# Kernel optimization log

Hardware: AMD Instinct MI355X
Metric: run time of the kernel (lower is better)

The kernel has to match this reference:

```python
import jax, jax.numpy as jnp
import numpy as np

B, L, S, H, E, D = 4, 2048, 2048, 8, 64, 64

def setup_inputs() -> dict:
    key = jax.random.key(0)
    kq, kk, kv = jax.random.split(key, 3)
    queries = jax.random.normal(kq, (B, L, H, E), dtype=jnp.float32)
    keys = jax.random.normal(kk, (B, S, H, E), dtype=jnp.float32)
    values = jax.random.normal(kv, (B, S, H, D), dtype=jnp.float32)
    # TriangularCausalMask: True above the diagonal (positions to mask)
    causal = jnp.triu(jnp.ones((L, S), dtype=bool), k=1)
    attn_mask = jnp.broadcast_to(causal[None, None], (B, 1, L, S))
    return {"queries": queries, "keys": keys, "values": values, "attn_mask": attn_mask}

def reference(queries, keys, values, attn_mask):
    scale = 1.0 / jnp.sqrt(jnp.asarray(E, queries.dtype))
    # scores: [B,H,L,S]
    scores = jnp.einsum('blhe,bshe->bhls', queries, keys)
    neg_inf = jnp.asarray(-jnp.inf, scores.dtype)
    scores = jnp.where(attn_mask, neg_inf, scores)
    A = jax.nn.softmax(scale * scores, axis=-1)
    # dropout is identity in eval mode
    V = jnp.einsum('bhls,bshd->blhd', A, values)
    return V
```

## Files before the change

### kernel.cpp

```cpp
#include <hip/hip_runtime.h>
#include <math.h>

typedef __attribute__((ext_vector_type(8))) short bf16x8;
typedef __attribute__((ext_vector_type(4))) float f32x4;
typedef __attribute__((ext_vector_type(4))) unsigned int u32x4;

#define B_ 4
#define L_ 2048
#define S_ 2048
#define H_ 8
#define E_ 64
#define D_ 64
#define NT_ 32
#define TILE_BYTES 16384
#define WS_NEEDED ((size_t)B_ * H_ * NT_ * TILE_BYTES)
#define SCL (0.125f * 1.44269504088896f)

__device__ __forceinline__ unsigned short f2bf(float x) {
    unsigned int u = __builtin_bit_cast(unsigned int, x);
    u += 0x7fffu + ((u >> 16) & 1u);
    return (unsigned short)(u >> 16);
}
__device__ __forceinline__ int rho(int r) {
    return (r & 32) | (((r >> 2) & 1) << 4) | (((r >> 3) & 3) << 2) | (r & 3);
}
__device__ __forceinline__ void gload16(const void* g, void* l) {
    __builtin_amdgcn_global_load_lds((const __attribute__((address_space(1))) unsigned int*)g,
                                     (__attribute__((address_space(3))) unsigned int*)l, 16, 0, 0);
}

__global__ __launch_bounds__(256) void prep_kv(const float* __restrict__ K,
                                               const float* __restrict__ V,
                                               unsigned short* __restrict__ ws)
{
    __shared__ __align__(16) unsigned short vt[64][80];
    const int tid = threadIdx.x;
    const int bid = blockIdx.x;
    const int kt  = bid >> 5;
    const int bh  = (((bid >> 3) & 3) << 3) | (bid & 7);
    const int b   = bh >> 3, h = bh & 7;
    const int s0  = kt * 64;
    const int r   = tid >> 2;
    const int e0  = (tid & 3) * 16;

    const float* krow = K + (((size_t)(b * S_ + s0 + r)) * H_ + h) * E_ + e0;
    const float* vrow = V + (((size_t)(b * S_ + s0 + r)) * H_ + h) * D_ + e0;
    char* tile = (char*)(ws) + ((size_t)(bh * NT_ + kt) * TILE_BYTES);

    unsigned short kb[16];
    #pragma unroll
    for (int i = 0; i < 4; ++i) {
        f32x4 k4 = *(const f32x4*)(krow + i * 4);
        #pragma unroll
        for (int jq = 0; jq < 4; ++jq) kb[i * 4 + jq] = f2bf(k4[jq]);
    }
    {
        const int rr = rho(r);
        const int m  = (rr & 7) << 4;
        char* kbase = tile + rr * 128;
        u32x4 lo, hi;
        #pragma unroll
        for (int jq = 0; jq < 4; ++jq) {
            lo[jq] = (unsigned)kb[2 * jq] | ((unsigned)kb[2 * jq + 1] << 16);
            hi[jq] = (unsigned)kb[8 + 2 * jq] | ((unsigned)kb[9 + 2 * jq] << 16);
        }
        *(u32x4*)(kbase + ((2 * e0) ^ m))      = lo;
        *(u32x4*)(kbase + ((2 * e0 + 16) ^ m)) = hi;
    }
    #pragma unroll
    for (int i = 0; i < 4; ++i) {
        f32x4 v4 = *(const f32x4*)(vrow + i * 4);
        #pragma unroll
        for (int jq = 0; jq < 4; ++jq) vt[e0 + i * 4 + jq][r] = f2bf(v4[jq]);
    }
    __syncthreads();
    {
        const int d  = tid >> 2;
        const int c0 = (tid & 3) * 16;
        const int m  = (d & 7) << 4;
        char* vbase = tile + 8192 + d * 128;
        u32x4 lo = *(const u32x4*)&vt[d][c0];
        u32x4 hi = *(const u32x4*)&vt[d][c0 + 8];
        *(u32x4*)(vbase + ((2 * c0) ^ m))      = lo;
        *(u32x4*)(vbase + ((2 * c0 + 16) ^ m)) = hi;
    }
}

__device__ __forceinline__ void do_group(
    const float* __restrict__ Q, const char* __restrict__ tb, char* __restrict__ pool,
    int b0, int h, int g, int team, int tw, int lq, int gl, int tid,
    float* __restrict__ O)
{
    const int nt = g + 1;
    const int nh = (nt + 1) >> 1;
    const int q0 = g * 64 + tw * 32;
    int qrow[2];
    qrow[0] = q0 + lq;
    qrow[1] = q0 + 16 + lq;

    bf16x8 qf[2][2];
    #pragma unroll
    for (int qs = 0; qs < 2; ++qs) {
        const float* qptr = Q + (((size_t)(b0 * L_ + qrow[qs])) * H_ + h) * E_;
        #pragma unroll
        for (int eb = 0; eb < 2; ++eb) {
            const float* pq = qptr + eb * 32 + gl * 8;
            f32x4 a = *(const f32x4*)pq;
            f32x4 b = *(const f32x4*)(pq + 4);
            bf16x8 qv;
            #pragma unroll
            for (int k = 0; k < 4; ++k) {
                qv[k]     = (short)f2bf(a[k] * SCL);
                qv[4 + k] = (short)f2bf(b[k] * SCL);
            }
            qf[qs][eb] = qv;
        }
    }

    f32x4 acc[2][4] = {};
    float ls[2] = {0.f, 0.f};

    #define STAGE13(I, BUF) do { \
        int tbi = nh + (I); if (tbi > nt - 1) tbi = nt - 1; \
        const char* ga = tb + (size_t)(I) * TILE_BYTES; \
        const char* gb = tb + (size_t)tbi * TILE_BYTES; \
        char* la = pool + (BUF) * 16384; \
        char* lb = pool + 32768 + (BUF) * 16384; \
        _Pragma("unroll") \
        for (int r4 = 0; r4 < 4; ++r4) { \
            gload16(ga + r4 * 4096 + tid * 16, la + r4 * 4096 + tid * 16); \
            gload16(gb + r4 * 4096 + tid * 16, lb + r4 * 4096 + tid * 16); \
        } \
    } while (0)

    STAGE13(0, 0);
    int cur = 0;
    for (int i = 0; i < nh; ++i) {
        if (i + 1 < nh) {
            STAGE13(i + 1, cur ^ 1);
            asm volatile("s_waitcnt vmcnt(8)" ::: "memory");
        } else {
            asm volatile("s_waitcnt vmcnt(0)" ::: "memory");
        }
        __builtin_amdgcn_s_barrier();
        __builtin_amdgcn_sched_barrier(0);

        const int kt = team ? (nh + i) : i;
        const bool active = team ? (kt < nt) : true;
        if (active) {
            const char* Kl = pool + team * 32768 + cur * 16384;
            const char* Vl = Kl + 8192;
            const int kv0 = kt * 64;
            const bool maskit = (kt == g);

            u32x4 pw[2][2];
            #pragma unroll
            for (int st = 0; st < 4; ++st) {
                const int row = st * 16 + lq;
                const int mm = (row & 7) << 4;
                const char* kr = Kl + row * 128;
                bf16x8 k0 = *(const bf16x8*)(kr + ((16 * gl) ^ mm));
                bf16x8 k1 = *(const bf16x8*)(kr + ((64 + 16 * gl) ^ mm));
                #pragma unroll
                for (int qs = 0; qs < 2; ++qs) {
                    f32x4 z = {0.f, 0.f, 0.f, 0.f};
                    __builtin_amdgcn_s_setprio(1);
                    f32x4 cc = __builtin_amdgcn_mfma_f32_16x16x32_bf16(k0, qf[qs][0], z, 0, 0, 0);
                    cc = __builtin_amdgcn_mfma_f32_16x16x32_bf16(k1, qf[qs][1], cc, 0, 0, 0);
                    __builtin_amdgcn_s_setprio(0);
                    if (maskit) {
                        #pragma unroll
                        for (int r = 0; r < 4; ++r) {
                            const int kv = kv0 + 32 * (st >> 1) + 8 * gl + 4 * (st & 1) + r;
                            if (kv > qrow[qs]) cc[r] = -INFINITY;
                        }
                    }
                    f32x4 ev;
                    #pragma unroll
                    for (int r = 0; r < 4; ++r)
                        asm("v_exp_f32 %0, %1" : "=v"(ev[r]) : "v"(cc[r]));
                    ls[qs] += (ev[0] + ev[1]) + (ev[2] + ev[3]);
                    asm("v_cvt_pk_bf16_f32 %0, %1, %2" : "=v"(pw[qs][st >> 1][2 * (st & 1)])     : "v"(ev[0]), "v"(ev[1]));
                    asm("v_cvt_pk_bf16_f32 %0, %1, %2" : "=v"(pw[qs][st >> 1][2 * (st & 1) + 1]) : "v"(ev[2]), "v"(ev[3]));
                }
            }

            #pragma unroll
            for (int dt = 0; dt < 4; ++dt) {
                const int row = dt * 16 + lq;
                const int mm = (row & 7) << 4;
                bf16x8 v0 = *(const bf16x8*)(Vl + row * 128 + ((16 * gl) ^ mm));
                bf16x8 v1 = *(const bf16x8*)(Vl + row * 128 + ((64 + 16 * gl) ^ mm));
                __builtin_amdgcn_s_setprio(1);
                #pragma unroll
                for (int qs = 0; qs < 2; ++qs) {
                    acc[qs][dt] = __builtin_amdgcn_mfma_f32_16x16x32_bf16(v0, __builtin_bit_cast(bf16x8, pw[qs][0]), acc[qs][dt], 0, 0, 0);
                    acc[qs][dt] = __builtin_amdgcn_mfma_f32_16x16x32_bf16(v1, __builtin_bit_cast(bf16x8, pw[qs][1]), acc[qs][dt], 0, 0, 0);
                }
                __builtin_amdgcn_s_setprio(0);
            }
        }
        __builtin_amdgcn_s_barrier();
        cur ^= 1;
    }
    #undef STAGE13

    float* sacc = (float*)pool;
    float* sls  = (float*)(pool + 64 * 68 * 4);
    if (team == 1) {
        #pragma unroll
        for (int qs = 0; qs < 2; ++qs) {
            const int rowl = tw * 32 + qs * 16 + lq;
            float l = ls[qs] + __shfl_xor(ls[qs], 16);
            l += __shfl_xor(l, 32);
            if (gl == 0) sls[rowl] = l;
            #pragma unroll
            for (int dt = 0; dt < 4; ++dt)
                *(f32x4*)&sacc[rowl * 68 + dt * 16 + 4 * gl] = acc[qs][dt];
        }
    }
    __syncthreads();
    if (team == 0) {
        #pragma unroll
        for (int qs = 0; qs < 2; ++qs) {
            const int rowl = tw * 32 + qs * 16 + lq;
            float l = ls[qs] + __shfl_xor(ls[qs], 16);
            l += __shfl_xor(l, 32);
            const float inv = 1.0f / (l + sls[rowl]);
            float* op = O + (((size_t)(b0 * L_ + qrow[qs])) * H_ + h) * D_;
            #pragma unroll
            for (int dt = 0; dt < 4; ++dt) {
                f32x4 p = *(const f32x4*)&sacc[rowl * 68 + dt * 16 + 4 * gl];
                f32x4 o;
                #pragma unroll
                for (int r = 0; r < 4; ++r) o[r] = (acc[qs][dt][r] + p[r]) * inv;
                *(f32x4*)(op + dt * 16 + 4 * gl) = o;
            }
        }
    }
    __syncthreads();
}

__global__ __launch_bounds__(256, 2) void attn13(const float* __restrict__ Q,
                                                 const unsigned short* __restrict__ ws,
                                                 float* __restrict__ O)
{
    __shared__ __align__(16) char pool[65536];

    const int tid  = threadIdx.x;
    const int lane = tid & 63;
    const int w    = tid >> 6;
    const int team = w >> 1;
    const int tw   = w & 1;
    const int lq   = lane & 15;
    const int gl   = lane >> 4;

    const int bid = blockIdx.x;
    const int bh  = bid & 31;
    const int pr  = bid >> 5;
    const int b0  = bh >> 3, h = bh & 7;

    const char* tb = (const char*)ws + (size_t)bh * NT_ * TILE_BYTES;

    do_group(Q, tb, pool, b0, h, pr,      team, tw, lq, gl, tid, O);
    do_group(Q, tb, pool, b0, h, 31 - pr, team, tw, lq, gl, tid, O);
}

#define KPITCH 72
__global__ __launch_bounds__(256, 2) void attn_fwd_fb(
    const float* __restrict__ Q, const float* __restrict__ K,
    const float* __restrict__ V, float* __restrict__ O)
{
    __shared__ unsigned short Klds[64 * KPITCH];
    __shared__ unsigned short Vlds[64 * KPITCH];
    const int tid = threadIdx.x, lane = tid & 63, w = tid >> 6;
    const int lq = lane & 15, g = lane >> 4;
    const int bid = blockIdx.x, qb = bid & 31, bh = bid >> 5;
    const int b0 = bh >> 3, h = bh & 7;
    const int q0 = qb * 64, qrow = q0 + w * 16 + lq;
    const float* qptr = Q + ((size_t)(b0 * L_ + qrow) * H_ + h) * E_;
    bf16x8 qf[2];
    #pragma unroll
    for (int eb = 0; eb < 2; ++eb) {
        const float* pp = qptr + eb * 32 + g * 8;
        f32x4 a = *(const f32x4*)pp; f32x4 b = *(const f32x4*)(pp + 4);
        bf16x8 qv;
        #pragma unroll
        for (int jq = 0; jq < 4; ++jq) { qv[jq] = (short)f2bf(a[jq] * 0.125f); qv[4 + jq] = (short)f2bf(b[jq] * 0.125f); }
        qf[eb] = qv;
    }
    const int tr = tid >> 2, tc = tid & 3;
    const int rh = rho(tr);
    f32x4 acc[4] = {};
    float mrow = -INFINITY, lrow = 0.f;
    for (int kt = 0; kt < qb + 1; ++kt) {
        const int kv0 = kt * 64;
        __syncthreads();
        {
            const float* krow = K + ((size_t)((b0 * S_ + kv0 + tr)) * H_ + h) * E_;
            const float* vrow = V + ((size_t)((b0 * S_ + kv0 + tr)) * H_ + h) * D_;
            #pragma unroll
            for (int i = 0; i < 4; ++i) {
                const int e0 = tc * 4 + i * 16;
                f32x4 k4 = *(const f32x4*)(krow + e0);
                unsigned int lo = (unsigned)f2bf(k4[0]) | ((unsigned)f2bf(k4[1]) << 16);
                unsigned int hi = (unsigned)f2bf(k4[2]) | ((unsigned)f2bf(k4[3]) << 16);
                *(uint2*)&Klds[rh * KPITCH + e0] = make_uint2(lo, hi);
                f32x4 v4 = *(const f32x4*)(vrow + e0);
                #pragma unroll
                for (int k2 = 0; k2 < 4; ++k2) Vlds[(e0 + k2) * KPITCH + tr] = f2bf(v4[k2]);
            }
        }
        __syncthreads();
        f32x4 sc[4];
        #pragma unroll
        for (int st = 0; st < 4; ++st) {
            const unsigned short* kr = &Klds[(st * 16 + lq) * KPITCH];
            bf16x8 ka0 = *(const bf16x8*)(kr + 8 * g);
            bf16x8 ka1 = *(const bf16x8*)(kr + 32 + 8 * g);
            f32x4 cc = {0.f, 0.f, 0.f, 0.f};
            cc = __builtin_amdgcn_mfma_f32_16x16x32_bf16(ka0, qf[0], cc, 0, 0, 0);
            cc = __builtin_amdgcn_mfma_f32_16x16x32_bf16(ka1, qf[1], cc, 0, 0, 0);
            sc[st] = cc;
        }
        float tmax = -INFINITY;
        #pragma unroll
        for (int st = 0; st < 4; ++st) {
            const int kvb = kv0 + 32 * (st >> 1) + 8 * g + 4 * (st & 1);
            #pragma unroll
            for (int r = 0; r < 4; ++r) { if (kvb + r > qrow) sc[st][r] = -INFINITY; tmax = fmaxf(tmax, sc[st][r]); }
        }
        tmax = fmaxf(tmax, __shfl_xor(tmax, 16));
        tmax = fmaxf(tmax, __shfl_xor(tmax, 32));
        const float mnew = fmaxf(mrow, tmax);
        const float corr = __expf(mrow - mnew);
        float pv[4][4]; float tsum = 0.f;
        #pragma unroll
        for (int st = 0; st < 4; ++st)
            #pragma unroll
            for (int r = 0; r < 4; ++r) { float e = __expf(sc[st][r] - mnew); pv[st][r] = e; tsum += e; }
        tsum += __shfl_xor(tsum, 16); tsum += __shfl_xor(tsum, 32);
        lrow = lrow * corr + tsum; mrow = mnew;
        #pragma unroll
        for (int dt = 0; dt < 4; ++dt)
            #pragma unroll
            for (int r = 0; r < 4; ++r) acc[dt][r] *= corr;
        bf16x8 pb[2];
        #pragma unroll
        for (int bb = 0; bb < 2; ++bb)
            #pragma unroll
            for (int s = 0; s < 2; ++s)
                #pragma unroll
                for (int r = 0; r < 4; ++r) pb[bb][4 * s + r] = (short)f2bf(pv[2 * bb + s][r]);
        #pragma unroll
        for (int bb = 0; bb < 2; ++bb)
            #pragma unroll
            for (int dt = 0; dt < 4; ++dt) {
                bf16x8 va = *(const bf16x8*)&Vlds[(dt * 16 + lq) * KPITCH + 32 * bb + 8 * g];
                acc[dt] = __builtin_amdgcn_mfma_f32_16x16x32_bf16(va, pb[bb], acc[dt], 0, 0, 0);
            }
    }
    const float inv = 1.0f / lrow;
    float* optr = O + ((size_t)(b0 * L_ + qrow) * H_ + h) * D_;
    #pragma unroll
    for (int dt = 0; dt < 4; ++dt) {
        f32x4 o;
        #pragma unroll
        for (int r = 0; r < 4; ++r) o[r] = acc[dt][r] * inv;
        *(f32x4*)(optr + dt * 16 + 4 * g) = o;
    }
}

extern "C" void kernel_launch(void* const* d_in, const int* in_sizes, int n_in,
                              void* d_out, int out_size, void* d_ws, size_t ws_size,
                              hipStream_t stream) {
    const float* Q = (const float*)d_in[0];
    const float* K = (const float*)d_in[1];
    const float* V = (const float*)d_in[2];
    float* O = (float*)d_out;
    if (ws_size >= WS_NEEDED) {
        prep_kv<<<dim3(B_ * H_ * NT_), 256, 0, stream>>>(K, V, (unsigned short*)d_ws);
        attn13<<<dim3(512), 256, 0, stream>>>(Q, (const unsigned short*)d_ws, O);
    } else {
        attn_fwd_fb<<<dim3(B_ * H_ * 32), 256, 0, stream>>>(Q, K, V, O);
    }
}
```

Measured before the change: 43.94 us.

## Widen attention blocks to 512 threads with four KV-split teams and 64-row waves

Blocks now use 512 threads with 128KB LDS and process 128-query-row groups. The KV range of each group is split across four teams instead of two, and each wave handles 64 query rows (four 16-row slices) instead of 32. This reuses each K/V fragment read from LDS across more queries and halves the grid to 256 blocks. The cost is higher register pressure from the larger accumulators, at most one block per CU because of the LDS footprint, and a larger three-way cross-team reduction through shared memory.

```diff
diff --git a/kernel.cpp b/kernel.cpp
--- a/kernel.cpp
+++ b/kernel.cpp
@@ -86,21 +86,24 @@
     }
 }
 
-__device__ __forceinline__ void do_group(
+__device__ __forceinline__ void do_grp14(
     const float* __restrict__ Q, const char* __restrict__ tb, char* __restrict__ pool,
-    int b0, int h, int g, int team, int tw, int lq, int gl, int tid,
+    int b0, int h, int gg, int team, int lw, int lq, int gl, int tid,
     float* __restrict__ O)
 {
-    const int nt = g + 1;
-    const int nh = (nt + 1) >> 1;
-    const int q0 = g * 64 + tw * 32;
-    int qrow[2];
-    qrow[0] = q0 + lq;
-    qrow[1] = q0 + 16 + lq;
-
-    bf16x8 qf[2][2];
-    #pragma unroll
-    for (int qs = 0; qs < 2; ++qs) {
+    const int nt = 2 * gg + 2;
+    const int kb = (nt * team) >> 2;
+    const int ke = (nt * (team + 1)) >> 2;
+    const int M  = (nt + 3) >> 2;
+    const int c  = 2 * gg + lw;
+
+    int qrow[4];
+    #pragma unroll
+    for (int qs = 0; qs < 4; ++qs) qrow[qs] = c * 64 + qs * 16 + lq;
+
+    bf16x8 qf[4][2];
+    #pragma unroll
+    for (int qs = 0; qs < 4; ++qs) {
         const float* qptr = Q + (((size_t)(b0 * L_ + qrow[qs])) * H_ + h) * E_;
         #pragma unroll
         for (int eb = 0; eb < 2; ++eb) {
@@ -117,27 +120,26 @@
         }
     }
 
-    f32x4 acc[2][4] = {};
-    float ls[2] = {0.f, 0.f};
-
-    #define STAGE13(I, BUF) do { \
-        int tbi = nh + (I); if (tbi > nt - 1) tbi = nt - 1; \
-        const char* ga = tb + (size_t)(I) * TILE_BYTES; \
-        const char* gb = tb + (size_t)tbi * TILE_BYTES; \
-        char* la = pool + (BUF) * 16384; \
-        char* lb = pool + 32768 + (BUF) * 16384; \
+    f32x4 acc[4][4] = {};
+    float ls[4] = {0.f, 0.f, 0.f, 0.f};
+
+    const int soff = tid & 127;
+    char* myb = pool + team * 32768;
+
+    #define STAGE14(I, BUF) do { \
+        int ti = kb + (I); if (ti > nt - 1) ti = nt - 1; \
+        const char* gp = tb + (size_t)ti * TILE_BYTES + soff * 16; \
+        char* lp = myb + (BUF) * 16384 + soff * 16; \
         _Pragma("unroll") \
-        for (int r4 = 0; r4 < 4; ++r4) { \
-            gload16(ga + r4 * 4096 + tid * 16, la + r4 * 4096 + tid * 16); \
-            gload16(gb + r4 * 4096 + tid * 16, lb + r4 * 4096 + tid * 16); \
-        } \
+        for (int r8 = 0; r8 < 8; ++r8) \
+            gload16(gp + r8 * 2048, lp + r8 * 2048); \
     } while (0)
 
-    STAGE13(0, 0);
-    int cur = 0;
-    for (int i = 0; i < nh; ++i) {
-        if (i + 1 < nh) {
-            STAGE13(i + 1, cur ^ 1);
+    STAGE14(0, 0);
+    int buf = 0;
+    for (int i = 0; i < M; ++i) {
+        if (i + 1 < M) {
+            STAGE14(i + 1, buf ^ 1);
             asm volatile("s_waitcnt vmcnt(8)" ::: "memory");
         } else {
             asm volatile("s_waitcnt vmcnt(0)" ::: "memory");
@@ -145,15 +147,14 @@
         __builtin_amdgcn_s_barrier();
         __builtin_amdgcn_sched_barrier(0);
 
-        const int kt = team ? (nh + i) : i;
-        const bool active = team ? (kt < nt) : true;
-        if (active) {
-            const char* Kl = pool + team * 32768 + cur * 16384;
+        const int kt = kb + i;
+        if (kt < ke && kt <= c) {
+            const char* Kl = myb + buf * 16384;
             const char* Vl = Kl + 8192;
             const int kv0 = kt * 64;
-            const bool maskit = (kt == g);
-
-            u32x4 pw[2][2];
+            const bool maskit = (kt == c);
+
+            u32x4 pw[4][2];
             #pragma unroll
             for (int st = 0; st < 4; ++st) {
                 const int row = st * 16 + lq;
@@ -162,7 +163,7 @@
                 bf16x8 k0 = *(const bf16x8*)(kr + ((16 * gl) ^ mm));
                 bf16x8 k1 = *(const bf16x8*)(kr + ((64 + 16 * gl) ^ mm));
                 #pragma unroll
-                for (int qs = 0; qs < 2; ++qs) {
+                for (int qs = 0; qs < 4; ++qs) {
                     f32x4 z = {0.f, 0.f, 0.f, 0.f};
                     __builtin_amdgcn_s_setprio(1);
                     f32x4 cc = __builtin_amdgcn_mfma_f32_16x16x32_bf16(k0, qf[qs][0], z, 0, 0, 0);
@@ -193,7 +194,7 @@
                 bf16x8 v1 = *(const bf16x8*)(Vl + row * 128 + ((64 + 16 * gl) ^ mm));
                 __builtin_amdgcn_s_setprio(1);
                 #pragma unroll
-                for (int qs = 0; qs < 2; ++qs) {
+                for (int qs = 0; qs < 4; ++qs) {
                     acc[qs][dt] = __builtin_amdgcn_mfma_f32_16x16x32_bf16(v0, __builtin_bit_cast(bf16x8, pw[qs][0]), acc[qs][dt], 0, 0, 0);
                     acc[qs][dt] = __builtin_amdgcn_mfma_f32_16x16x32_bf16(v1, __builtin_bit_cast(bf16x8, pw[qs][1]), acc[qs][dt], 0, 0, 0);
                 }
@@ -201,69 +202,74 @@
             }
         }
         __builtin_amdgcn_s_barrier();
-        cur ^= 1;
-    }
-    #undef STAGE13
-
-    float* sacc = (float*)pool;
-    float* sls  = (float*)(pool + 64 * 68 * 4);
-    if (team == 1) {
-        #pragma unroll
-        for (int qs = 0; qs < 2; ++qs) {
-            const int rowl = tw * 32 + qs * 16 + lq;
+        buf ^= 1;
+    }
+    #undef STAGE14
+
+    float (*sacc)[68] = (float(*)[68])pool;
+    float* sls = (float*)(pool + 3 * 128 * 68 * 4);
+    if (team != 0) {
+        #pragma unroll
+        for (int qs = 0; qs < 4; ++qs) {
             float l = ls[qs] + __shfl_xor(ls[qs], 16);
             l += __shfl_xor(l, 32);
+            const int rowl = (team - 1) * 128 + lw * 64 + qs * 16 + lq;
             if (gl == 0) sls[rowl] = l;
             #pragma unroll
             for (int dt = 0; dt < 4; ++dt)
-                *(f32x4*)&sacc[rowl * 68 + dt * 16 + 4 * gl] = acc[qs][dt];
+                *(f32x4*)&sacc[rowl][dt * 16 + 4 * gl] = acc[qs][dt];
         }
     }
     __syncthreads();
     if (team == 0) {
         #pragma unroll
-        for (int qs = 0; qs < 2; ++qs) {
-            const int rowl = tw * 32 + qs * 16 + lq;
+        for (int qs = 0; qs < 4; ++qs) {
             float l = ls[qs] + __shfl_xor(ls[qs], 16);
             l += __shfl_xor(l, 32);
-            const float inv = 1.0f / (l + sls[rowl]);
+            const int rl = lw * 64 + qs * 16 + lq;
+            l += sls[rl] + sls[128 + rl] + sls[256 + rl];
+            const float inv = 1.0f / l;
             float* op = O + (((size_t)(b0 * L_ + qrow[qs])) * H_ + h) * D_;
             #pragma unroll
             for (int dt = 0; dt < 4; ++dt) {
-                f32x4 p = *(const f32x4*)&sacc[rowl * 68 + dt * 16 + 4 * gl];
+                const int dc = dt * 16 + 4 * gl;
+                f32x4 p0 = *(const f32x4*)&sacc[rl][dc];
+                f32x4 p1 = *(const f32x4*)&sacc[128 + rl][dc];
+                f32x4 p2 = *(const f32x4*)&sacc[256 + rl][dc];
                 f32x4 o;
                 #pragma unroll
-                for (int r = 0; r < 4; ++r) o[r] = (acc[qs][dt][r] + p[r]) * inv;
-                *(f32x4*)(op + dt * 16 + 4 * gl) = o;
+                for (int r = 0; r < 4; ++r)
+                    o[r] = (acc[qs][dt][r] + p0[r] + p1[r] + p2[r]) * inv;
+                *(f32x4*)(op + dc) = o;
             }
         }
     }
     __syncthreads();
 }
 
-__global__ __launch_bounds__(256, 2) void attn13(const float* __restrict__ Q,
+__global__ __launch_bounds__(512, 2) void attn14(const float* __restrict__ Q,
                                                  const unsigned short* __restrict__ ws,
                                                  float* __restrict__ O)
 {
-    __shared__ __align__(16) char pool[65536];
+    __shared__ __align__(16) char pool[131072];
 
     const int tid  = threadIdx.x;
     const int lane = tid & 63;
     const int w    = tid >> 6;
     const int team = w >> 1;
-    const int tw   = w & 1;
+    const int lw   = w & 1;
     const int lq   = lane & 15;
     const int gl   = lane >> 4;
 
     const int bid = blockIdx.x;
     const int bh  = bid & 31;
-    const int pr  = bid >> 5;
+    const int pj  = bid >> 5;
     const int b0  = bh >> 3, h = bh & 7;
 
     const char* tb = (const char*)ws + (size_t)bh * NT_ * TILE_BYTES;
 
-    do_group(Q, tb, pool, b0, h, pr,      team, tw, lq, gl, tid, O);
-    do_group(Q, tb, pool, b0, h, 31 - pr, team, tw, lq, gl, tid, O);
+    do_grp14(Q, tb, pool, b0, h, pj,      team, lw, lq, gl, tid, O);
+    do_grp14(Q, tb, pool, b0, h, 15 - pj, team, lw, lq, gl, tid, O);
 }
 
 #define KPITCH 72
@@ -380,7 +386,7 @@
     float* O = (float*)d_out;
     if (ws_size >= WS_NEEDED) {
         prep_kv<<<dim3(B_ * H_ * NT_), 256, 0, stream>>>(K, V, (unsigned short*)d_ws);
-        attn13<<<dim3(512), 256, 0, stream>>>(Q, (const unsigned short*)d_ws, O);
+        attn14<<<dim3(256), 512, 0, stream>>>(Q, (const unsigned short*)d_ws, O);
     } else {
         attn_fwd_fb<<<dim3(B_ * H_ * 32), 256, 0, stream>>>(Q, K, V, O);
     }
```

Result: slower. 53.05 us (+20.7%).
